# Optimization experiments

Hardware: AMD Instinct MI355X
Metric: run time of the kernel (lower is better)

## Reference

```python
import jax, jax.numpy as jnp
import numpy as np

ALPHA = 0.2  # LeakyReLU negative slope
NEG_INF = -9e15


def setup_inputs() -> dict:
    key = jax.random.key(0)
    ks = jax.random.split(key, 6)
    B, N, F_in, F_out = 16, 1024, 1024, 512
    x = jax.random.normal(ks[0], (B, N, F_in), dtype=jnp.float32)
    adj = jax.random.randint(ks[1], (B, N, N), 0, 2, dtype=jnp.int32)
    W = jax.random.normal(ks[2], (F_in, F_out), dtype=jnp.float32) * 0.02
    a = jax.random.normal(ks[3], (2 * F_out, 1), dtype=jnp.float32) * 0.02
    fc_w = jax.random.normal(ks[4], (F_out, 2 * F_out), dtype=jnp.float32) * 0.02
    fc_b = jnp.zeros((F_out,), dtype=jnp.float32)
    return {"x": x, "adj": adj, "W": W, "a": a, "fc_w": fc_w, "fc_b": fc_b}


def reference(x, adj, W, a, fc_w, fc_b):
    # h: [B, N, F_out]
    h = jnp.matmul(x, W)
    F_out = W.shape[1]
    # The original builds a_input = concat(h_i, h_j) of shape [B,N,N,2F] and
    # contracts with a. Equivalently (same math, no O(N^2 F) intermediate):
    # e_ij = leakyrelu(h_i . a[:F] + h_j . a[F:])
    a1 = a[:F_out, 0]  # [F_out]
    a2 = a[F_out:, 0]  # [F_out]
    f1 = jnp.einsum('bnf,f->bn', h, a1)  # source term
    f2 = jnp.einsum('bnf,f->bn', h, a2)  # target term
    e = jax.nn.leaky_relu(f1[:, :, None] + f2[:, None, :], negative_slope=ALPHA)  # [B,N,N]
    attention = jnp.where(adj > 0, e, jnp.full_like(e, NEG_INF))
    attention = jax.nn.softmax(attention, axis=2)
    # dropout is identity in eval mode
    agg = jnp.matmul(attention, h)  # [B,N,F_out]
    h_prime = jnp.concatenate([agg, h], axis=2)  # [B,N,2F]
    h_prime = jnp.matmul(h_prime, fc_w.T) + fc_b
    return jax.nn.elu(h_prime)  # concat=True path
```

## Files before the change

kernel.cpp:

```cpp
#include <hip/hip_runtime.h>

#define ALPHA 0.2f

typedef __attribute__((ext_vector_type(8))) short short8;
typedef __attribute__((ext_vector_type(4))) float f32x4;

__device__ __forceinline__ unsigned short f2b(float f) {
  unsigned int u; __builtin_memcpy(&u, &f, 4);
  unsigned int r = (u + 0x7FFFu + ((u >> 16) & 1u)) >> 16;
  return (unsigned short)r;
}
__device__ __forceinline__ float b2f(unsigned short v) {
  unsigned int u = ((unsigned int)v) << 16; float f; __builtin_memcpy(&f, &u, 4); return f;
}
__device__ __forceinline__ void gl_lds16(const unsigned short* g, unsigned short* l) {
  __builtin_amdgcn_global_load_lds((__attribute__((address_space(1))) void*)g,
                                   (__attribute__((address_space(3))) void*)l, 16, 0, 0);
}
__device__ __forceinline__ uint4 pack8(float4 v0, float4 v1) {
  alignas(16) unsigned short o[8];
  o[0] = f2b(v0.x); o[1] = f2b(v0.y); o[2] = f2b(v0.z); o[3] = f2b(v0.w);
  o[4] = f2b(v1.x); o[5] = f2b(v1.y); o[6] = f2b(v1.z); o[7] = f2b(v1.w);
  return *(const uint4*)o;
}

__device__ __forceinline__ void cvt_f4(const float* __restrict__ in,
                                       unsigned short* __restrict__ out,
                                       unsigned int f4idx) {
  float4 v = ((const float4*)in)[f4idx];
  alignas(8) unsigned short o[4];
  o[0] = f2b(v.x); o[1] = f2b(v.y); o[2] = f2b(v.z); o[3] = f2b(v.w);
  ((uint2*)out)[f4idx] = *(const uint2*)o;
}

__global__ __launch_bounds__(256) void prep1(const float* __restrict__ fcw,
                                             unsigned short* __restrict__ fcwb,
                                             const float* __restrict__ W,
                                             unsigned short* __restrict__ Wt) {
  __shared__ alignas(16) unsigned short tile[64][72];
  unsigned int bx = blockIdx.x;
  unsigned int tid = threadIdx.x;
  if (bx < 256u) {
    unsigned int base = bx * 512u;
    cvt_f4(fcw, fcwb, base + tid);
    cvt_f4(fcw, fcwb, base + 256u + tid);
  } else {
    unsigned int idx = bx - 256u;
    unsigned int k0 = (idx >> 3) * 64, n0 = (idx & 7) * 64;
    #pragma unroll
    for (int p = 0; p < 4; p++) {
      int r = p * 16 + (tid >> 4);
      int c = (tid & 15) * 4;
      float4 v = *(const float4*)(W + (size_t)(k0 + r) * 512 + n0 + c);
      tile[r][c] = f2b(v.x); tile[r][c + 1] = f2b(v.y);
      tile[r][c + 2] = f2b(v.z); tile[r][c + 3] = f2b(v.w);
    }
    __syncthreads();
    int f = tid >> 2;
    int ic = (tid & 3) * 16;
    alignas(16) unsigned short buf[16];
    #pragma unroll
    for (int k = 0; k < 16; k++) buf[k] = tile[ic + k][f];
    uint4* dst = (uint4*)(Wt + (size_t)(n0 + f) * 1024 + k0 + ic);
    dst[0] = ((const uint4*)buf)[0];
    dst[1] = ((const uint4*)buf)[1];
  }
}

__global__ __launch_bounds__(256) void prep2(const unsigned short* __restrict__ hp,
                                             const float* __restrict__ a,
                                             float* __restrict__ f1, float* __restrict__ f2,
                                             unsigned short* __restrict__ ht) {
  __shared__ alignas(16) unsigned short tile[64][72];
  int bx = blockIdx.x;
  int tid = threadIdx.x;
  if (bx < 4096) {
    int row = bx * 4 + (tid >> 6);
    int lane = tid & 63;
    const unsigned short* hrow = hp + (size_t)row * 1024 + 512;
    uint4 raw = *(const uint4*)(hrow + lane * 8);
    alignas(16) unsigned short hv[8]; __builtin_memcpy(hv, &raw, 16);
    float s1 = 0.f, s2 = 0.f;
    #pragma unroll
    for (int j = 0; j < 8; j++) {
      float hf = b2f(hv[j]);
      s1 += hf * a[lane * 8 + j];
      s2 += hf * a[512 + lane * 8 + j];
    }
    #pragma unroll
    for (int o = 32; o > 0; o >>= 1) { s1 += __shfl_down(s1, o); s2 += __shfl_down(s2, o); }
    if (lane == 0) { f1[row] = s1; f2[row] = s2; }
  } else {
    int idx = bx - 4096;
    int b = idx >> 7;
    int f0 = ((idx >> 4) & 7) * 64;
    int i0 = (idx & 15) * 64;
    #pragma unroll
    for (int p = 0; p < 2; p++) {
      int r = p * 32 + (tid >> 3);
      int c = (tid & 7) * 8;
      uint4 v = *(const uint4*)(hp + (size_t)(b * 1024 + i0 + r) * 1024 + 512 + f0 + c);
      *(uint4*)(&tile[r][c]) = v;
    }
    __syncthreads();
    int f = tid >> 2;
    int ic = (tid & 3) * 16;
    alignas(16) unsigned short buf[16];
    #pragma unroll
    for (int k = 0; k < 16; k++) buf[k] = tile[ic + k][f];
    uint4* dst = (uint4*)(ht + (size_t)(b * 512 + f0 + f) * 1024 + i0 + ic);
    dst[0] = ((const uint4*)buf)[0];
    dst[1] = ((const uint4*)buf)[1];
  }
}

__global__ __launch_bounds__(256) void rowsum_P(const int* __restrict__ adj,
                                                const float* __restrict__ f1,
                                                const float* __restrict__ f2,
                                                float* __restrict__ invl,
                                                unsigned short* __restrict__ P) {
  int row = blockIdx.x * 4 + (threadIdx.x >> 6);
  int lane = threadIdx.x & 63;
  int b = row >> 10;
  float f1v = f1[row];
  const int4* ap = (const int4*)(adj + (size_t)row * 1024) + lane * 4;
  int4 a0 = ap[0];
  int4 a1 = ap[1];
  int4 a2 = ap[2];
  int4 a3 = ap[3];
  int av[16] = {a0.x, a0.y, a0.z, a0.w, a1.x, a1.y, a1.z, a1.w,
                a2.x, a2.y, a2.z, a2.w, a3.x, a3.y, a3.z, a3.w};
  const float* f2p = f2 + (b << 10) + lane * 16;
  float4 v0 = ((const float4*)f2p)[0];
  float4 v1 = ((const float4*)f2p)[1];
  float4 v2 = ((const float4*)f2p)[2];
  float4 v3 = ((const float4*)f2p)[3];
  float fv[16] = {v0.x, v0.y, v0.z, v0.w, v1.x, v1.y, v1.z, v1.w,
                  v2.x, v2.y, v2.z, v2.w, v3.x, v3.y, v3.z, v3.w};
  float s = 0.f;
  alignas(16) unsigned short o[16];
  #pragma unroll
  for (int j = 0; j < 16; j++) {
    float p = 0.f;
    if (av[j] > 0) {
      float z = f1v + fv[j];
      z = z > 0.f ? z : ALPHA * z;
      p = __expf(z);
      s += p;
    }
    o[j] = f2b(p);
  }
  uint4* dst = (uint4*)(P + (size_t)row * 1024 + lane * 16);
  dst[0] = ((const uint4*)o)[0];
  dst[1] = ((const uint4*)o)[1];
  #pragma unroll
  for (int off = 32; off > 0; off >>= 1) s += __shfl_down(s, off);
  if (lane == 0) invl[row] = 1.0f / s;
}

template <int EPI, int CVTA>
__global__ __launch_bounds__(256) void gemm_bt(
    const void* __restrict__ A_, size_t aBS,
    const unsigned short* __restrict__ Bt, size_t bBS,
    int K,
    void* __restrict__ outp, size_t oBS, int ldo, int ocol,
    const float* __restrict__ scale,
    const float* __restrict__ bias) {
  __shared__ alignas(16) unsigned short As[2 * 128 * 64];
  __shared__ alignas(16) unsigned short Bs[2 * 128 * 64];
  const int tid = threadIdx.x;
  const int lane = tid & 63;
  const int w = tid >> 6;
  const int m0 = blockIdx.x * 128;
  const int n0 = blockIdx.y * 128;
  const int zb = blockIdx.z;
  const unsigned short* Btb = Bt + (size_t)zb * bBS;

  f32x4 acc[4][4];
  #pragma unroll
  for (int i = 0; i < 4; i++)
    #pragma unroll
    for (int j = 0; j < 4; j++)
      #pragma unroll
      for (int r = 0; r < 4; r++) acc[i][j][r] = 0.f;

  const int lr = lane >> 3;
  const int lc = (lane & 7) ^ (lr & 7);
  const unsigned short* ag = nullptr;
  const float* agf = nullptr;
  if (CVTA)
    agf = (const float*)A_ + (size_t)zb * aBS + (size_t)(m0 + w * 32 + lr) * K + lc * 8;
  else
    ag = (const unsigned short*)A_ + (size_t)zb * aBS + (size_t)(m0 + w * 32 + lr) * K + lc * 8;
  const unsigned short* bg = Btb + (size_t)(n0 + w * 32 + lr) * K + lc * 8;
  const int sbase = w * 32 * 64;
  const int lofs = lane * 8;

  const int wm = (w & 1) * 64;
  const int wn = (w >> 1) * 64;
  const int row16 = lane & 15;
  const int quad = lane >> 4;
  const int sw = row16 & 7;

  if (CVTA) {
    float4 av[4][2];
    #pragma unroll
    for (int t = 0; t < 4; t++) {
      av[t][0] = *(const float4*)(agf + (size_t)(t * 8) * K);
      av[t][1] = *(const float4*)(agf + (size_t)(t * 8) * K + 4);
    }
    #pragma unroll
    for (int t = 0; t < 4; t++)
      gl_lds16(bg + (size_t)(t * 8) * K, Bs + sbase + t * 512);
    #pragma unroll
    for (int t = 0; t < 4; t++)
      *(uint4*)(As + sbase + t * 512 + lofs) = pack8(av[t][0], av[t][1]);
  } else {
    #pragma unroll
    for (int t = 0; t < 4; t++) {
      gl_lds16(ag + (size_t)(t * 8) * K, As + sbase + t * 512);
      gl_lds16(bg + (size_t)(t * 8) * K, Bs + sbase + t * 512);
    }
  }
  __syncthreads();

  int bufo = 0;
  for (int k0 = 0; k0 < K; k0 += 64) {
    const int nbufo = bufo ^ 8192;
    const bool pf = (k0 + 64 < K);
    float4 av[4][2];
    if (pf) {
      if (CVTA) {
        #pragma unroll
        for (int t = 0; t < 4; t++) {
          av[t][0] = *(const float4*)(agf + (k0 + 64) + (size_t)(t * 8) * K);
          av[t][1] = *(const float4*)(agf + (k0 + 64) + (size_t)(t * 8) * K + 4);
        }
      } else {
        #pragma unroll
        for (int t = 0; t < 4; t++)
          gl_lds16(ag + (k0 + 64) + (size_t)(t * 8) * K, As + nbufo + sbase + t * 512);
      }
      #pragma unroll
      for (int t = 0; t < 4; t++)
        gl_lds16(bg + (k0 + 64) + (size_t)(t * 8) * K, Bs + nbufo + sbase + t * 512);
    }
    short8 af[2][4], bf[2][4];
    #pragma unroll
    for (int s = 0; s < 2; s++) {
      #pragma unroll
      for (int i = 0; i < 4; i++) {
        af[s][i] = *(const short8*)(As + bufo + (wm + i * 16 + row16) * 64 + ((s * 4 + quad) ^ sw) * 8);
        bf[s][i] = *(const short8*)(Bs + bufo + (wn + i * 16 + row16) * 64 + ((s * 4 + quad) ^ sw) * 8);
      }
    }
    #pragma unroll
    for (int s = 0; s < 2; s++)
      #pragma unroll
      for (int am = 0; am < 4; am++)
        #pragma unroll
        for (int bn = 0; bn < 4; bn++)
          acc[am][bn] = __builtin_amdgcn_mfma_f32_16x16x32_bf16(af[s][am], bf[s][bn], acc[am][bn], 0, 0, 0);
    if (pf && CVTA) {
      #pragma unroll
      for (int t = 0; t < 4; t++)
        *(uint4*)(As + nbufo + sbase + t * 512 + lofs) = pack8(av[t][0], av[t][1]);
    }
    __syncthreads();
    bufo = nbufo;
  }

  const int col = lane & 15;
  const int r0 = quad * 4;
  #pragma unroll
  for (int am = 0; am < 4; am++) {
    #pragma unroll
    for (int bn = 0; bn < 4; bn++) {
      #pragma unroll
      for (int r = 0; r < 4; r++) {
        int m = m0 + wm + am * 16 + r0 + r;
        int n = n0 + wn + bn * 16 + col;
        float v = acc[am][bn][r];
        if (EPI == 3) v *= scale[zb * 1024 + m];
        if (EPI == 2) {
          v += bias[n];
          v = v > 0.f ? v : expm1f(v);
          ((float*)outp)[(size_t)m * ldo + n] = v;
        } else {
          ((unsigned short*)outp)[(size_t)zb * oBS + (size_t)m * ldo + ocol + n] = f2b(v);
        }
      }
    }
  }
}

extern "C" void kernel_launch(void* const* d_in, const int* in_sizes, int n_in,
                              void* d_out, int out_size, void* d_ws, size_t ws_size,
                              hipStream_t stream) {
  const float* x   = (const float*)d_in[0];
  const int*   adj = (const int*)d_in[1];
  const float* W   = (const float*)d_in[2];
  const float* a   = (const float*)d_in[3];
  const float* fcw = (const float*)d_in[4];
  const float* fcb = (const float*)d_in[5];
  float* out = (float*)d_out;
  char* ws = (char*)d_ws;

  unsigned short* P    = (unsigned short*)(ws);
  unsigned short* hp   = (unsigned short*)(ws + 33554432);
  unsigned short* ht   = (unsigned short*)(ws + 67108864);
  unsigned short* Wt   = (unsigned short*)(ws + 83886080);
  unsigned short* fcwb = (unsigned short*)(ws + 84934656);
  float* f1            = (float*)(ws + 85983232);
  float* f2            = (float*)(ws + 86048768);
  float* invl          = (float*)(ws + 86114304);

  prep1<<<384, 256, 0, stream>>>(fcw, fcwb, W, Wt);

  gemm_bt<1, 1><<<dim3(128, 4, 1), 256, 0, stream>>>(x, 0, Wt, 0, 1024,
                                                     hp, 0, 1024, 512, nullptr, nullptr);
  prep2<<<6144, 256, 0, stream>>>(hp, a, f1, f2, ht);
  rowsum_P<<<4096, 256, 0, stream>>>(adj, f1, f2, invl, P);

  gemm_bt<3, 0><<<dim3(8, 4, 16), 256, 0, stream>>>(P, 1024 * 1024, ht, 512 * 1024, 1024,
                                                    hp, 1024 * 1024, 1024, 0, invl, nullptr);
  gemm_bt<2, 0><<<dim3(128, 4, 1), 256, 0, stream>>>(hp, 0, fcwb, 0, 1024,
                                                     out, 0, 512, 0, nullptr, fcb);
}
```

Baseline: 260.2 us.

## Use 8 waves per GEMM block with 64x32 warp tiles

```diff
diff --git a/kernel.cpp b/kernel.cpp
--- a/kernel.cpp
+++ b/kernel.cpp
@@ -159,7 +159,7 @@
 }
 
 template <int EPI, int CVTA>
-__global__ __launch_bounds__(256) void gemm_bt(
+__global__ __launch_bounds__(512, 4) void gemm_bt(
     const void* __restrict__ A_, size_t aBS,
     const unsigned short* __restrict__ Bt, size_t bBS,
     int K,
@@ -176,11 +176,11 @@
   const int zb = blockIdx.z;
   const unsigned short* Btb = Bt + (size_t)zb * bBS;
 
-  f32x4 acc[4][4];
+  f32x4 acc[4][2];
   #pragma unroll
   for (int i = 0; i < 4; i++)
     #pragma unroll
-    for (int j = 0; j < 4; j++)
+    for (int j = 0; j < 2; j++)
       #pragma unroll
       for (int r = 0; r < 4; r++) acc[i][j][r] = 0.f;
 
@@ -189,38 +189,36 @@
   const unsigned short* ag = nullptr;
   const float* agf = nullptr;
   if (CVTA)
-    agf = (const float*)A_ + (size_t)zb * aBS + (size_t)(m0 + w * 32 + lr) * K + lc * 8;
+    agf = (const float*)A_ + (size_t)zb * aBS + (size_t)(m0 + w * 8 + lr) * K + lc * 8;
   else
-    ag = (const unsigned short*)A_ + (size_t)zb * aBS + (size_t)(m0 + w * 32 + lr) * K + lc * 8;
-  const unsigned short* bg = Btb + (size_t)(n0 + w * 32 + lr) * K + lc * 8;
-  const int sbase = w * 32 * 64;
+    ag = (const unsigned short*)A_ + (size_t)zb * aBS + (size_t)(m0 + w * 8 + lr) * K + lc * 8;
+  const unsigned short* bg = Btb + (size_t)(n0 + w * 8 + lr) * K + lc * 8;
+  const int sb0 = (w * 8) * 64;
+  const int sb1 = (64 + w * 8) * 64;
   const int lofs = lane * 8;
 
   const int wm = (w & 1) * 64;
-  const int wn = (w >> 1) * 64;
+  const int wn = (w >> 1) * 32;
   const int row16 = lane & 15;
   const int quad = lane >> 4;
   const int sw = row16 & 7;
 
   if (CVTA) {
-    float4 av[4][2];
-    #pragma unroll
-    for (int t = 0; t < 4; t++) {
-      av[t][0] = *(const float4*)(agf + (size_t)(t * 8) * K);
-      av[t][1] = *(const float4*)(agf + (size_t)(t * 8) * K + 4);
-    }
-    #pragma unroll
-    for (int t = 0; t < 4; t++)
-      gl_lds16(bg + (size_t)(t * 8) * K, Bs + sbase + t * 512);
-    #pragma unroll
-    for (int t = 0; t < 4; t++)
-      *(uint4*)(As + sbase + t * 512 + lofs) = pack8(av[t][0], av[t][1]);
+    float4 av[2][2];
+    #pragma unroll
+    for (int t = 0; t < 2; t++) {
+      av[t][0] = *(const float4*)(agf + (size_t)(t * 64) * K);
+      av[t][1] = *(const float4*)(agf + (size_t)(t * 64) * K + 4);
+    }
+    gl_lds16(bg, Bs + sb0);
+    gl_lds16(bg + (size_t)64 * K, Bs + sb1);
+    *(uint4*)(As + sb0 + lofs) = pack8(av[0][0], av[0][1]);
+    *(uint4*)(As + sb1 + lofs) = pack8(av[1][0], av[1][1]);
   } else {
-    #pragma unroll
-    for (int t = 0; t < 4; t++) {
-      gl_lds16(ag + (size_t)(t * 8) * K, As + sbase + t * 512);
-      gl_lds16(bg + (size_t)(t * 8) * K, Bs + sbase + t * 512);
-    }
+    gl_lds16(ag, As + sb0);
+    gl_lds16(ag + (size_t)64 * K, As + sb1);
+    gl_lds16(bg, Bs + sb0);
+    gl_lds16(bg + (size_t)64 * K, Bs + sb1);
   }
   __syncthreads();
 
@@ -228,43 +226,41 @@
   for (int k0 = 0; k0 < K; k0 += 64) {
     const int nbufo = bufo ^ 8192;
     const bool pf = (k0 + 64 < K);
-    float4 av[4][2];
+    float4 av[2][2];
     if (pf) {
       if (CVTA) {
         #pragma unroll
-        for (int t = 0; t < 4; t++) {
-          av[t][0] = *(const float4*)(agf + (k0 + 64) + (size_t)(t * 8) * K);
-          av[t][1] = *(const float4*)(agf + (k0 + 64) + (size_t)(t * 8) * K + 4);
+        for (int t = 0; t < 2; t++) {
+          av[t][0] = *(const float4*)(agf + (k0 + 64) + (size_t)(t * 64) * K);
+          av[t][1] = *(const float4*)(agf + (k0 + 64) + (size_t)(t * 64) * K + 4);
         }
       } else {
-        #pragma unroll
-        for (int t = 0; t < 4; t++)
-          gl_lds16(ag + (k0 + 64) + (size_t)(t * 8) * K, As + nbufo + sbase + t * 512);
+        gl_lds16(ag + (k0 + 64), As + nbufo + sb0);
+        gl_lds16(ag + (k0 + 64) + (size_t)64 * K, As + nbufo + sb1);
       }
-      #pragma unroll
-      for (int t = 0; t < 4; t++)
-        gl_lds16(bg + (k0 + 64) + (size_t)(t * 8) * K, Bs + nbufo + sbase + t * 512);
-    }
-    short8 af[2][4], bf[2][4];
+      gl_lds16(bg + (k0 + 64), Bs + nbufo + sb0);
+      gl_lds16(bg + (k0 + 64) + (size_t)64 * K, Bs + nbufo + sb1);
+    }
+    short8 af[2][4], bf[2][2];
     #pragma unroll
     for (int s = 0; s < 2; s++) {
       #pragma unroll
-      for (int i = 0; i < 4; i++) {
+      for (int i = 0; i < 4; i++)
         af[s][i] = *(const short8*)(As + bufo + (wm + i * 16 + row16) * 64 + ((s * 4 + quad) ^ sw) * 8);
-        bf[s][i] = *(const short8*)(Bs + bufo + (wn + i * 16 + row16) * 64 + ((s * 4 + quad) ^ sw) * 8);
-      }
+      #pragma unroll
+      for (int j = 0; j < 2; j++)
+        bf[s][j] = *(const short8*)(Bs + bufo + (wn + j * 16 + row16) * 64 + ((s * 4 + quad) ^ sw) * 8);
     }
     #pragma unroll
     for (int s = 0; s < 2; s++)
       #pragma unroll
       for (int am = 0; am < 4; am++)
         #pragma unroll
-        for (int bn = 0; bn < 4; bn++)
+        for (int bn = 0; bn < 2; bn++)
           acc[am][bn] = __builtin_amdgcn_mfma_f32_16x16x32_bf16(af[s][am], bf[s][bn], acc[am][bn], 0, 0, 0);
     if (pf && CVTA) {
-      #pragma unroll
-      for (int t = 0; t < 4; t++)
-        *(uint4*)(As + nbufo + sbase + t * 512 + lofs) = pack8(av[t][0], av[t][1]);
+      *(uint4*)(As + nbufo + sb0 + lofs) = pack8(av[0][0], av[0][1]);
+      *(uint4*)(As + nbufo + sb1 + lofs) = pack8(av[1][0], av[1][1]);
     }
     __syncthreads();
     bufo = nbufo;
@@ -275,7 +271,7 @@
   #pragma unroll
   for (int am = 0; am < 4; am++) {
     #pragma unroll
-    for (int bn = 0; bn < 4; bn++) {
+    for (int bn = 0; bn < 2; bn++) {
       #pragma unroll
       for (int r = 0; r < 4; r++) {
         int m = m0 + wm + am * 16 + r0 + r;
@@ -317,13 +313,13 @@
 
   prep1<<<384, 256, 0, stream>>>(fcw, fcwb, W, Wt);
 
-  gemm_bt<1, 1><<<dim3(128, 4, 1), 256, 0, stream>>>(x, 0, Wt, 0, 1024,
+  gemm_bt<1, 1><<<dim3(128, 4, 1), 512, 0, stream>>>(x, 0, Wt, 0, 1024,
                                                      hp, 0, 1024, 512, nullptr, nullptr);
   prep2<<<6144, 256, 0, stream>>>(hp, a, f1, f2, ht);
   rowsum_P<<<4096, 256, 0, stream>>>(adj, f1, f2, invl, P);
 
-  gemm_bt<3, 0><<<dim3(8, 4, 16), 256, 0, stream>>>(P, 1024 * 1024, ht, 512 * 1024, 1024,
+  gemm_bt<3, 0><<<dim3(8, 4, 16), 512, 0, stream>>>(P, 1024 * 1024, ht, 512 * 1024, 1024,
                                                     hp, 1024 * 1024, 1024, 0, invl, nullptr);
-  gemm_bt<2, 0><<<dim3(128, 4, 1), 256, 0, stream>>>(hp, 0, fcwb, 0, 1024,
+  gemm_bt<2, 0><<<dim3(128, 4, 1), 512, 0, stream>>>(hp, 0, fcwb, 0, 1024,
                                                      out, 0, 512, 0, nullptr, fcb);
 }
```

After: 251.7 us. 1.03x faster.
